# Performance work log

Measured on AMD Instinct MI355X. Metric: run time of the kernel, lower is better.

The kernel has to match this reference:

```python
import jax, jax.numpy as jnp
import numpy as np

N, M, NNZ, D, H = 4096, 1024, 65536, 512, 8
DH = D // H
DFF = 4 * D
EPS = 1e-5


def layer_norm(x, g, b):
    mu = jnp.mean(x, axis=-1, keepdims=True)
    var = jnp.mean((x - mu) ** 2, axis=-1, keepdims=True)
    return (x - mu) / jnp.sqrt(var + EPS) * g + b


def setup_inputs() -> dict:
    key = jax.random.key(0)
    ks = jax.random.split(key, 16)
    s = 1.0 / np.sqrt(D)
    inp = {}
    inp['x'] = jax.random.normal(ks[0], (N, D), jnp.float32)
    node = jax.random.randint(ks[1], (NNZ,), 0, N, jnp.int32)
    edge = jax.random.randint(ks[2], (NNZ,), 0, M, jnp.int32)
    inp['hyperedge_index'] = jnp.stack([node, edge], axis=0)
    inp['hyperedge_attr'] = jax.random.normal(ks[3], (M, D), jnp.float32)
    # HypergraphConv params (heads=1): lin (no bias), att [2*D], output bias
    inp['Wh'] = jax.random.normal(ks[4], (D, D), jnp.float32) * s
    inp['att'] = jax.random.normal(ks[5], (2 * D,), jnp.float32) * s
    inp['bias_h'] = jnp.zeros((D,), jnp.float32)
    # outer LayerNorms
    inp['ln1_g'] = jnp.ones((D,), jnp.float32); inp['ln1_b'] = jnp.zeros((D,), jnp.float32)
    inp['ln2_g'] = jnp.ones((D,), jnp.float32); inp['ln2_b'] = jnp.zeros((D,), jnp.float32)
    # TransformerEncoderLayer params (post-norm, relu, dropout off at eval)
    inp['in_proj_w'] = jax.random.normal(ks[6], (3 * D, D), jnp.float32) * s
    inp['in_proj_b'] = jnp.zeros((3 * D,), jnp.float32)
    inp['out_proj_w'] = jax.random.normal(ks[7], (D, D), jnp.float32) * s
    inp['out_proj_b'] = jnp.zeros((D,), jnp.float32)
    inp['ff1_w'] = jax.random.normal(ks[8], (DFF, D), jnp.float32) * s
    inp['ff1_b'] = jnp.zeros((DFF,), jnp.float32)
    inp['ff2_w'] = jax.random.normal(ks[9], (D, DFF), jnp.float32) * (1.0 / np.sqrt(DFF))
    inp['ff2_b'] = jnp.zeros((D,), jnp.float32)
    inp['tln1_g'] = jnp.ones((D,), jnp.float32); inp['tln1_b'] = jnp.zeros((D,), jnp.float32)
    inp['tln2_g'] = jnp.ones((D,), jnp.float32); inp['tln2_b'] = jnp.zeros((D,), jnp.float32)
    return inp


def hypergraph_conv(x, node, edge, hyperedge_attr, Wh, att, bias_h):
    # PyG HypergraphConv, use_attention=True, heads=1, concat=True
    xl = x @ Wh.T                      # [N, D]
    el = hyperedge_attr @ Wh.T         # [M, D]
    # per-incidence attention score
    a = xl[node] @ att[:D] + el[edge] @ att[D:]          # [NNZ]
    a = jnp.where(a >= 0, a, 0.2 * a)                    # leaky_relu(0.2)
    # scatter-softmax grouped by node index
    amax = jax.ops.segment_max(a, node, num_segments=N)
    a = jnp.exp(a - amax[node])
    den = jax.ops.segment_sum(a, node, num_segments=N)
    alpha = a / (den[node] + 1e-16)
    # degree normalizations (hyperedge_weight = ones)
    ones = jnp.ones((NNZ,), x.dtype)
    Dn = jax.ops.segment_sum(ones, node, num_segments=N)
    Dinv = jnp.where(Dn > 0, 1.0 / Dn, 0.0)
    Bn = jax.ops.segment_sum(ones, edge, num_segments=M)
    Binv = jnp.where(Bn > 0, 1.0 / Bn, 0.0)
    # node -> hyperedge aggregation
    msg1 = (Binv[edge] * alpha)[:, None] * xl[node]      # [NNZ, D]
    ef = jax.ops.segment_sum(msg1, edge, num_segments=M)  # [M, D]
    # hyperedge -> node aggregation
    msg2 = (Dinv[node] * alpha)[:, None] * ef[edge]
    out = jax.ops.segment_sum(msg2, node, num_segments=N)  # [N, D]
    return out + bias_h


def reference(x, hyperedge_index, hyperedge_attr, Wh, att, bias_h,
              ln1_g, ln1_b, ln2_g, ln2_b,
              in_proj_w, in_proj_b, out_proj_w, out_proj_b,
              ff1_w, ff1_b, ff2_w, ff2_b,
              tln1_g, tln1_b, tln2_g, tln2_b):
    node, edge = hyperedge_index[0], hyperedge_index[1]
    x_conv = hypergraph_conv(x, node, edge, hyperedge_attr, Wh, att, bias_h)
    x1 = layer_norm(x + x_conv, ln1_g, ln1_b)
    # TransformerEncoderLayer (post-norm, eval: dropout off), seq of N tokens
    qkv = x1 @ in_proj_w.T + in_proj_b
    q, k, v = jnp.split(qkv, 3, axis=-1)
    q = q.reshape(N, H, DH); k = k.reshape(N, H, DH); v = v.reshape(N, H, DH)
    scores = jnp.einsum('nhd,mhd->hnm', q, k) / np.sqrt(DH)
    attw = jax.nn.softmax(scores, axis=-1)
    ctx = jnp.einsum('hnm,mhd->nhd', attw, v).reshape(N, D)
    attn_out = ctx @ out_proj_w.T + out_proj_b
    x2 = layer_norm(x1 + attn_out, tln1_g, tln1_b)
    ff = jax.nn.relu(x2 @ ff1_w.T + ff1_b) @ ff2_w.T + ff2_b
    x3 = layer_norm(x2 + ff, tln2_g, tln2_b)
    return layer_norm(x1 + x3, ln2_g, ln2_b)
```

## Files before the change

kernel.cpp:

```cpp
#include <hip/hip_runtime.h>
#include <math.h>

#define NN   4096
#define MM   1024
#define NNZC 65536
#define DD   512
#define HH   8
#define DHH  64
#define DFFC 2048
#define NSPLIT 4

typedef short bf16x8 __attribute__((ext_vector_type(8)));
typedef float f32x4  __attribute__((ext_vector_type(4)));

static __device__ inline unsigned short f2bf(float f) {
  union { float f; unsigned int u; } v; v.f = f;
  unsigned int r = v.u + 0x7fff + ((v.u >> 16) & 1);
  return (unsigned short)(r >> 16);
}
static __device__ inline float bf2f(unsigned short u) {
  return __uint_as_float((unsigned int)u << 16);
}

__device__ inline void gload16(const void* g, void* l) {
  __builtin_amdgcn_global_load_lds(
      (const __attribute__((address_space(1))) void*)g,
      (__attribute__((address_space(3))) void*)l, 16, 0, 0);
}

__device__ inline void atomicMaxF(float* addr, float val) {
  if (val >= 0.f) atomicMax((int*)addr, __float_as_int(val));
  else            atomicMin((unsigned int*)addr, __float_as_uint(val));
}

__global__ void init_kernel(float* amax, float* den, int* DnCnt, int* BnCnt,
                            int* node_cur, int* edge_cur) {
  int i = blockIdx.x * 256 + threadIdx.x;
  if (i < NN) { amax[i] = -INFINITY; den[i] = 0.f; DnCnt[i] = 0; node_cur[i] = 0; }
  if (i < MM) { BnCnt[i] = 0; edge_cur[i] = 0; }
}

__global__ __launch_bounds__(256) void f2b_multi(
    const float* s0, unsigned short* d0, int n0,
    const float* s1, unsigned short* d1, int n1,
    const float* s2, unsigned short* d2, int n2,
    const float* s3, unsigned short* d3, int n3,
    const float* s4, unsigned short* d4, int n4,
    const float* s5, unsigned short* d5, int n5,
    const float* s6, unsigned short* d6, int n6) {
  const float* in; unsigned short* out; int n8;
  switch (blockIdx.y) {
    case 0: in=s0; out=d0; n8=n0; break;
    case 1: in=s1; out=d1; n8=n1; break;
    case 2: in=s2; out=d2; n8=n2; break;
    case 3: in=s3; out=d3; n8=n3; break;
    case 4: in=s4; out=d4; n8=n4; break;
    case 5: in=s5; out=d5; n8=n5; break;
    default: in=s6; out=d6; n8=n6; break;
  }
  for (int i = blockIdx.x*256 + threadIdx.x; i < n8; i += gridDim.x*256) {
    float4 v0 = *(const float4*)&in[(size_t)i*8];
    float4 v1 = *(const float4*)&in[(size_t)i*8 + 4];
    unsigned short w[8];
    w[0]=f2bf(v0.x); w[1]=f2bf(v0.y); w[2]=f2bf(v0.z); w[3]=f2bf(v0.w);
    w[4]=f2bf(v1.x); w[5]=f2bf(v1.y); w[6]=f2bf(v1.z); w[7]=f2bf(v1.w);
    *(ulonglong2*)&out[(size_t)i*8] = *(ulonglong2*)w;
  }
}

__global__ __launch_bounds__(256) void gemm_bt_bf16(
    const unsigned short* __restrict__ A, const unsigned short* __restrict__ B,
    const float* __restrict__ bias, float* __restrict__ Cf,
    unsigned short* __restrict__ Cb, int N, int K, int relu) {
  __shared__ __align__(16) unsigned short Al[128*64];
  __shared__ __align__(16) unsigned short Bl[128*64];
  const int t = threadIdx.x;
  const int w = t >> 6, l = t & 63;
  const int lg = l >> 4, lid = l & 15;
  const int wr = w >> 1, wc = w & 1;
  const int bm = blockIdx.x * 128, bn = blockIdx.y * 128;

  f32x4 acc[4][4];
  #pragma unroll
  for (int mi = 0; mi < 4; ++mi)
    #pragma unroll
    for (int ni = 0; ni < 4; ++ni) acc[mi][ni] = (f32x4)0.f;

  for (int k0 = 0; k0 < K; k0 += 64) {
    #pragma unroll
    for (int i = 0; i < 4; ++i) {
      int cid = i*256 + t;
      int row = cid >> 3, cp = cid & 7;
      int gc = cp ^ (row & 7);
      gload16(&A[(size_t)(bm + row)*K + k0 + gc*8], &Al[cid*8]);
      gload16(&B[(size_t)(bn + row)*K + k0 + gc*8], &Bl[cid*8]);
    }
    asm volatile("s_waitcnt vmcnt(0)" ::: "memory");
    __syncthreads();
    #pragma unroll
    for (int ks = 0; ks < 2; ++ks) {
      bf16x8 af[4], bfr[4];
      #pragma unroll
      for (int mi = 0; mi < 4; ++mi) {
        int r = wr*64 + mi*16 + lid;
        af[mi] = *(const bf16x8*)&Al[r*64 + ((ks*4 + lg) ^ (r & 7))*8];
      }
      #pragma unroll
      for (int ni = 0; ni < 4; ++ni) {
        int r = wc*64 + ni*16 + lid;
        bfr[ni] = *(const bf16x8*)&Bl[r*64 + ((ks*4 + lg) ^ (r & 7))*8];
      }
      __builtin_amdgcn_s_setprio(1);
      #pragma unroll
      for (int mi = 0; mi < 4; ++mi)
        #pragma unroll
        for (int ni = 0; ni < 4; ++ni)
          acc[mi][ni] = __builtin_amdgcn_mfma_f32_16x16x32_bf16(af[mi], bfr[ni], acc[mi][ni], 0, 0, 0);
      __builtin_amdgcn_s_setprio(0);
    }
    __syncthreads();
  }

  #pragma unroll
  for (int ni = 0; ni < 4; ++ni) {
    int col = bn + wc*64 + ni*16 + lid;
    float bv = bias ? bias[col] : 0.f;
    #pragma unroll
    for (int mi = 0; mi < 4; ++mi) {
      #pragma unroll
      for (int rg = 0; rg < 4; ++rg) {
        int row = bm + wr*64 + mi*16 + lg*4 + rg;
        float v = acc[mi][ni][rg] + bv;
        if (relu) v = fmaxf(v, 0.f);
        if (Cf) Cf[(size_t)row*N + col] = v;
        if (Cb) Cb[(size_t)row*N + col] = f2bf(v);
      }
    }
  }
}

__global__ __launch_bounds__(256) void gemm_bt_bf16_n64(
    const unsigned short* __restrict__ A, const unsigned short* __restrict__ B,
    const float* __restrict__ bias, unsigned short* __restrict__ Cb, int N, int K) {
  __shared__ __align__(16) unsigned short Al[128*64];
  __shared__ __align__(16) unsigned short Bl[64*64];
  const int t = threadIdx.x;
  const int w = t >> 6, l = t & 63;
  const int lg = l >> 4, lid = l & 15;
  const int wr = w >> 1, wc = w & 1;
  const int bm = blockIdx.x * 128, bn = blockIdx.y * 64;

  f32x4 acc[4][2];
  #pragma unroll
  for (int mi = 0; mi < 4; ++mi)
    #pragma unroll
    for (int ni = 0; ni < 2; ++ni) acc[mi][ni] = (f32x4)0.f;

  for (int k0 = 0; k0 < K; k0 += 64) {
    #pragma unroll
    for (int i = 0; i < 4; ++i) {
      int cid = i*256 + t;
      int row = cid >> 3, cp = cid & 7;
      int gc = cp ^ (row & 7);
      gload16(&A[(size_t)(bm + row)*K + k0 + gc*8], &Al[cid*8]);
    }
    #pragma unroll
    for (int i = 0; i < 2; ++i) {
      int cid = i*256 + t;
      int row = cid >> 3, cp = cid & 7;
      int gc = cp ^ (row & 7);
      gload16(&B[(size_t)(bn + row)*K + k0 + gc*8], &Bl[cid*8]);
    }
    asm volatile("s_waitcnt vmcnt(0)" ::: "memory");
    __syncthreads();
    #pragma unroll
    for (int ks = 0; ks < 2; ++ks) {
      bf16x8 af[4], bfr[2];
      #pragma unroll
      for (int mi = 0; mi < 4; ++mi) {
        int r = wr*64 + mi*16 + lid;
        af[mi] = *(const bf16x8*)&Al[r*64 + ((ks*4 + lg) ^ (r & 7))*8];
      }
      #pragma unroll
      for (int ni = 0; ni < 2; ++ni) {
        int r = wc*32 + ni*16 + lid;
        bfr[ni] = *(const bf16x8*)&Bl[r*64 + ((ks*4 + lg) ^ (r & 7))*8];
      }
      __builtin_amdgcn_s_setprio(1);
      #pragma unroll
      for (int mi = 0; mi < 4; ++mi)
        #pragma unroll
        for (int ni = 0; ni < 2; ++ni)
          acc[mi][ni] = __builtin_amdgcn_mfma_f32_16x16x32_bf16(af[mi], bfr[ni], acc[mi][ni], 0, 0, 0);
      __builtin_amdgcn_s_setprio(0);
    }
    __syncthreads();
  }

  #pragma unroll
  for (int ni = 0; ni < 2; ++ni) {
    int col = bn + wc*32 + ni*16 + lid;
    float bv = bias ? bias[col] : 0.f;
    #pragma unroll
    for (int mi = 0; mi < 4; ++mi) {
      #pragma unroll
      for (int rg = 0; rg < 4; ++rg) {
        int row = bm + wr*64 + mi*16 + lg*4 + rg;
        Cb[(size_t)row*N + col] = f2bf(acc[mi][ni][rg] + bv);
      }
    }
  }
}

__global__ __launch_bounds__(256) void rowdot_b16(const unsigned short* __restrict__ X,
    const float* __restrict__ vec, float* __restrict__ out, int rows) {
  int w = (blockIdx.x * 256 + threadIdx.x) >> 6;
  int lane = threadIdx.x & 63;
  if (w >= rows) return;
  const unsigned short* xr = &X[(size_t)w * DD];
  float s = 0.f;
  #pragma unroll
  for (int j = 0; j < 8; ++j) s += bf2f(xr[lane + 64*j]) * vec[lane + 64*j];
  #pragma unroll
  for (int off = 1; off < 64; off <<= 1) s += __shfl_xor(s, off, 64);
  if (lane == 0) out[w] = s;
}

__global__ void incidence_pass1(const int* __restrict__ node_idx, const int* __restrict__ edge_idx,
    const float* __restrict__ s_node, const float* __restrict__ s_edge,
    float* __restrict__ a_buf, float* amax, int* DnCnt, int* BnCnt) {
  int i = blockIdx.x * 256 + threadIdx.x;
  if (i >= NNZC) return;
  int n = node_idx[i], m = edge_idx[i];
  float a = s_node[n] + s_edge[m];
  a = (a >= 0.f) ? a : 0.2f * a;
  a_buf[i] = a;
  atomicMaxF(&amax[n], a);
  atomicAdd(&DnCnt[n], 1);
  atomicAdd(&BnCnt[m], 1);
}

__global__ __launch_bounds__(1024) void exscan_kernel(const int* __restrict__ in,
                                                      int* __restrict__ out, int n) {
  __shared__ int sums[1024];
  const int t = threadIdx.x;
  const int chunk = (n + 1023) >> 10;
  const int start = t * chunk;
  const int stop  = min(start + chunk, n);
  int local = 0;
  for (int i = start; i < stop; ++i) local += in[i];
  sums[t] = local;
  __syncthreads();
  for (int o = 1; o < 1024; o <<= 1) {
    int v = (t >= o) ? sums[t - o] : 0;
    __syncthreads();
    sums[t] += v;
    __syncthreads();
  }
  int run = (t == 0) ? 0 : sums[t - 1];
  for (int i = start; i < stop; ++i) { out[i] = run; run += in[i]; }
  if (t == 1023) out[n] = sums[1023];
}

__global__ void incidence_pass2(const int* __restrict__ node_idx, const int* __restrict__ edge_idx,
    float* __restrict__ a_buf, const float* __restrict__ amax, float* den,
    const int* __restrict__ node_off, const int* __restrict__ edge_off,
    int* node_cur, int* edge_cur, int* node_list, int* edge_list) {
  int i = blockIdx.x * 256 + threadIdx.x;
  if (i >= NNZC) return;
  int n = node_idx[i], m = edge_idx[i];
  float e = __expf(a_buf[i] - amax[n]);
  a_buf[i] = e;
  atomicAdd(&den[n], e);
  int pn = atomicAdd(&node_cur[n], 1);
  node_list[node_off[n] + pn] = i;
  int pm = atomicAdd(&edge_cur[m], 1);
  edge_list[edge_off[m] + pm] = i;
}

__global__ __launch_bounds__(256) void gather_edge(const int* __restrict__ edge_off,
    const int* __restrict__ edge_list, const int* __restrict__ node_idx,
    const float* __restrict__ a_buf, const float* __restrict__ den,
    const unsigned short* __restrict__ xlb, unsigned short* __restrict__ efb) {
  int m = blockIdx.x;
  int t = threadIdx.x;
  int beg = edge_off[m], end = edge_off[m+1];
  int cnt = end - beg;
  float Binv = (cnt > 0) ? (1.0f / (float)cnt) : 0.f;
  __shared__ int   ln_[128];
  __shared__ float lw_[128];
  float acc0 = 0.f, acc1 = 0.f;
  for (int c = beg; c < end; c += 128) {
    int nchunk = min(128, end - c);
    if (t < nchunk) {
      int i = edge_list[c + t];
      int n = node_idx[i];
      ln_[t] = n;
      lw_[t] = a_buf[i] / (den[n] + 1e-16f) * Binv;
    }
    __syncthreads();
    float a0 = 0.f, a1 = 0.f, b0 = 0.f, b1 = 0.f;
    int j = 0;
    for (; j + 1 < nchunk; j += 2) {
      float w0 = lw_[j], w1 = lw_[j+1];
      const unsigned short* r0 = &xlb[(size_t)ln_[j]   * DD];
      const unsigned short* r1 = &xlb[(size_t)ln_[j+1] * DD];
      a0 += w0 * bf2f(r0[t]);       b0 += w0 * bf2f(r0[t + 256]);
      a1 += w1 * bf2f(r1[t]);       b1 += w1 * bf2f(r1[t + 256]);
    }
    if (j < nchunk) {
      float w0 = lw_[j];
      const unsigned short* r0 = &xlb[(size_t)ln_[j] * DD];
      a0 += w0 * bf2f(r0[t]);       b0 += w0 * bf2f(r0[t + 256]);
    }
    acc0 += a0 + a1;
    acc1 += b0 + b1;
    __syncthreads();
  }
  efb[(size_t)m * DD + t]       = f2bf(acc0);
  efb[(size_t)m * DD + t + 256] = f2bf(acc1);
}

__global__ __launch_bounds__(256) void gather_node(const int* __restrict__ node_off,
    const int* __restrict__ node_list, const int* __restrict__ edge_idx,
    const float* __restrict__ a_buf, const float* __restrict__ den,
    const unsigned short* __restrict__ efb, const float* __restrict__ bias_h,
    float* __restrict__ conv) {
  int n = blockIdx.x;
  int t = threadIdx.x;
  int beg = node_off[n], end = node_off[n+1];
  int cnt = end - beg;
  float Dinv = (cnt > 0) ? (1.0f / (float)cnt) : 0.f;
  float wscale = Dinv / (den[n] + 1e-16f);
  __shared__ int   le_[128];
  __shared__ float lw_[128];
  float acc0 = 0.f, acc1 = 0.f;
  for (int c = beg; c < end; c += 128) {
    int nchunk = min(128, end - c);
    if (t < nchunk) {
      int i = node_list[c + t];
      le_[t] = edge_idx[i];
      lw_[t] = a_buf[i] * wscale;
    }
    __syncthreads();
    float a0 = 0.f, a1 = 0.f, b0 = 0.f, b1 = 0.f;
    int j = 0;
    for (; j + 1 < nchunk; j += 2) {
      float w0 = lw_[j], w1 = lw_[j+1];
      const unsigned short* r0 = &efb[(size_t)le_[j]   * DD];
      const unsigned short* r1 = &efb[(size_t)le_[j+1] * DD];
      a0 += w0 * bf2f(r0[t]);       b0 += w0 * bf2f(r0[t + 256]);
      a1 += w1 * bf2f(r1[t]);       b1 += w1 * bf2f(r1[t + 256]);
    }
    if (j < nchunk) {
      float w0 = lw_[j];
      const unsigned short* r0 = &efb[(size_t)le_[j] * DD];
      a0 += w0 * bf2f(r0[t]);       b0 += w0 * bf2f(r0[t + 256]);
    }
    acc0 += a0 + a1;
    acc1 += b0 + b1;
    __syncthreads();
  }
  conv[(size_t)n * DD + t]       = acc0 + bias_h[t];
  conv[(size_t)n * DD + t + 256] = acc1 + bias_h[t + 256];
}

__global__ __launch_bounds__(256) void ln_residual(const float* __restrict__ a,
    const float* __restrict__ b, const unsigned short* __restrict__ bB,
    const float* __restrict__ g, const float* __restrict__ be,
    float* __restrict__ out, unsigned short* __restrict__ outb) {
  int r = blockIdx.x;
  int t = threadIdx.x;
  float b0 = b ? b[(size_t)r*DD + t]       : bf2f(bB[(size_t)r*DD + t]);
  float b1 = b ? b[(size_t)r*DD + t + 256] : bf2f(bB[(size_t)r*DD + t + 256]);
  float v0 = a[(size_t)r*DD + t]       + b0;
  float v1 = a[(size_t)r*DD + t + 256] + b1;
  __shared__ float red[4];
  __shared__ float mu_s, rstd_s;
  float s = v0 + v1;
  #pragma unroll
  for (int off = 1; off < 64; off <<= 1) s += __shfl_xor(s, off, 64);
  int wid = t >> 6;
  if ((t & 63) == 0) red[wid] = s;
  __syncthreads();
  if (t == 0) mu_s = (red[0] + red[1] + red[2] + red[3]) / 512.f;
  __syncthreads();
  float mu = mu_s;
  float d0 = v0 - mu, d1 = v1 - mu;
  float vs = d0*d0 + d1*d1;
  #pragma unroll
  for (int off = 1; off < 64; off <<= 1) vs += __shfl_xor(vs, off, 64);
  if ((t & 63) == 0) red[wid] = vs;
  __syncthreads();
  if (t == 0) rstd_s = rsqrtf((red[0] + red[1] + red[2] + red[3]) / 512.f + 1e-5f);
  __syncthreads();
  float rs = rstd_s;
  float o0 = d0 * rs * g[t]       + be[t];
  float o1 = d1 * rs * g[t + 256] + be[t + 256];
  out[(size_t)r*DD + t]       = o0;
  out[(size_t)r*DD + t + 256] = o1;
  if (outb) {
    outb[(size_t)r*DD + t]       = f2bf(o0);
    outb[(size_t)r*DD + t + 256] = f2bf(o1);
  }
}

__global__ __launch_bounds__(256) void ln_final2(const float* __restrict__ x2,
    const unsigned short* __restrict__ ffob, const float* __restrict__ x1,
    const float* __restrict__ g1, const float* __restrict__ b1,
    const float* __restrict__ g2, const float* __restrict__ b2,
    float* __restrict__ out) {
  int r = blockIdx.x;
  int t = threadIdx.x;
  __shared__ float red[4];
  __shared__ float sh0, sh1;
  int wid = t >> 6;
  float v0 = x2[(size_t)r*DD + t]       + bf2f(ffob[(size_t)r*DD + t]);
  float v1 = x2[(size_t)r*DD + t + 256] + bf2f(ffob[(size_t)r*DD + t + 256]);
  float s = v0 + v1;
  #pragma unroll
  for (int off = 1; off < 64; off <<= 1) s += __shfl_xor(s, off, 64);
  if ((t & 63) == 0) red[wid] = s;
  __syncthreads();
  if (t == 0) sh0 = (red[0] + red[1] + red[2] + red[3]) / 512.f;
  __syncthreads();
  float mu = sh0;
  float d0 = v0 - mu, d1 = v1 - mu;
  float vs = d0*d0 + d1*d1;
  #pragma unroll
  for (int off = 1; off < 64; off <<= 1) vs += __shfl_xor(vs, off, 64);
  if ((t & 63) == 0) red[wid] = vs;
  __syncthreads();
  if (t == 0) sh1 = rsqrtf((red[0] + red[1] + red[2] + red[3]) / 512.f + 1e-5f);
  __syncthreads();
  float rs = sh1;
  float x30 = d0 * rs * g1[t]       + b1[t];
  float x31 = d1 * rs * g1[t + 256] + b1[t + 256];
  __syncthreads();
  float u0 = x1[(size_t)r*DD + t]       + x30;
  float u1 = x1[(size_t)r*DD + t + 256] + x31;
  s = u0 + u1;
  #pragma unroll
  for (int off = 1; off < 64; off <<= 1) s += __shfl_xor(s, off, 64);
  if ((t & 63) == 0) red[wid] = s;
  __syncthreads();
  if (t == 0) sh0 = (red[0] + red[1] + red[2] + red[3]) / 512.f;
  __syncthreads();
  mu = sh0;
  d0 = u0 - mu; d1 = u1 - mu;
  vs = d0*d0 + d1*d1;
  #pragma unroll
  for (int off = 1; off < 64; off <<= 1) vs += __shfl_xor(vs, off, 64);
  if ((t & 63) == 0) red[wid] = vs;
  __syncthreads();
  if (t == 0) sh1 = rsqrtf((red[0] + red[1] + red[2] + red[3]) / 512.f + 1e-5f);
  __syncthreads();
  rs = sh1;
  out[(size_t)r*DD + t]       = d0 * rs * g2[t]       + b2[t];
  out[(size_t)r*DD + t + 256] = d1 * rs * g2[t + 256] + b2[t + 256];
}

__global__ __launch_bounds__(256) void conv_vt(const unsigned short* __restrict__ qkvbb,
                                               unsigned short* __restrict__ Vtb) {
  __shared__ unsigned short Tl[64][76];
  const int h = blockIdx.y;
  const int tt = blockIdx.x * 64;
  const int t = threadIdx.x;
  {
    int row = t >> 2;
    int cbase = (t & 3) * 16;
    const unsigned short* src = &qkvbb[(size_t)(tt + row)*1536 + 1024 + h*64];
    #pragma unroll
    for (int jj = 0; jj < 4; ++jj)
      *(ushort4*)&Tl[row][cbase + jj*4] = *(const ushort4*)&src[cbase + jj*4];
  }
  __syncthreads();
  #pragma unroll
  for (int it = 0; it < 4; ++it) {
    int d = it*16 + (t >> 4);
    int tk = (t & 15) * 4;
    ushort4 w4;
    w4.x = Tl[tk+0][d]; w4.y = Tl[tk+1][d]; w4.z = Tl[tk+2][d]; w4.w = Tl[tk+3][d];
    *(ushort4*)&Vtb[(size_t)h*64*NN + (size_t)d*NN + tt + tk] = w4;
  }
}

__global__ __launch_bounds__(256) void attn_mfma_part(const unsigned short* __restrict__ qkvbb,
                                                      const unsigned short* __restrict__ Vtb,
                                                      unsigned short* __restrict__ Opartb,
                                                      float* __restrict__ ml) {
  const int head = blockIdx.y;
  const int z = blockIdx.z;
  const int q0 = blockIdx.x * 64;
  const int t = threadIdx.x;
  const int w = t >> 6;
  const int l = t & 63;
  const int lg = l >> 4;
  const int lid = l & 15;
  const float sc = 0.125f * 1.44269504f;
  const float THRraw = 44.36f;

  __shared__ __align__(16) unsigned short Kl[64*64];
  __shared__ __align__(16) unsigned short Vl[64*64];

  bf16x8 qa[2];
  {
    const int qrow = q0 + w*16 + lid;
    const unsigned short* qp = &qkvbb[(size_t)qrow*1536 + head*64];
    qa[0] = *(const bf16x8*)&qp[lg*8];
    qa[1] = *(const bf16x8*)&qp[32 + lg*8];
  }

  float m = -1e30f, msc = -1e30f, lsum = 0.f;
  f32x4 o[4];
  #pragma unroll
  for (int dt = 0; dt < 4; ++dt) o[dt] = (f32x4)0.f;

  const unsigned short* Kh = qkvbb + 512 + head*64;
  const unsigned short* Vh = Vtb + (size_t)head*64*NN;
  const int kt0 = z * (NN / NSPLIT);
  const int kt1 = kt0 + (NN / NSPLIT);

  const int srow0 = t >> 3,        scc = (t & 7) * 8;
  const int srow1 = 32 + (t >> 3);
  const int sdst0 = (srow0*64 + scc) ^ ((srow0 & 7) << 3);
  const int sdst1 = (srow1*64 + scc) ^ ((srow1 & 7) << 3);
  const int kperm0 = 8*((srow0>>2)&3) + 4*((srow0>>4)&1) + (srow0&3) + 32*(srow0>>5);
  const int kperm1 = 8*((srow1>>2)&3) + 4*((srow1>>4)&1) + (srow1&3) + 32*(srow1>>5);
  ulonglong2 kreg0, kreg1, vreg0, vreg1;

#define LOADKV(ktv) do { \
    kreg0 = *(const ulonglong2*)&Kh[(size_t)((ktv) + kperm0)*1536 + scc]; \
    vreg0 = *(const ulonglong2*)&Vh[(size_t)srow0*NN + (ktv) + scc]; \
    kreg1 = *(const ulonglong2*)&Kh[(size_t)((ktv) + kperm1)*1536 + scc]; \
    vreg1 = *(const ulonglong2*)&Vh[(size_t)srow1*NN + (ktv) + scc]; \
  } while (0)
#define STORKV() do { \
    *(ulonglong2*)&Kl[sdst0] = kreg0; *(ulonglong2*)&Vl[sdst0] = vreg0; \
    *(ulonglong2*)&Kl[sdst1] = kreg1; *(ulonglong2*)&Vl[sdst1] = vreg1; \
  } while (0)

  LOADKV(kt0);
  STORKV();
  __syncthreads();

  for (int kt = kt0; kt < kt1; kt += 64) {
    const bool hn = (kt + 64) < kt1;
    if (hn) LOADKV(kt + 64);

    f32x4 s[4];
    #pragma unroll
    for (int n = 0; n < 4; ++n) s[n] = (f32x4)0.f;
    __builtin_amdgcn_s_setprio(1);
    #pragma unroll
    for (int n = 0; n < 4; ++n) {
      int tok = n*16 + lid;
      #pragma unroll
      for (int hf = 0; hf < 2; ++hf) {
        int didx = (tok*64 + hf*32 + lg*8) ^ ((tok & 7) << 3);
        bf16x8 kb = *(const bf16x8*)&Kl[didx];
        s[n] = __builtin_amdgcn_mfma_f32_16x16x32_bf16(kb, qa[hf], s[n], 0, 0, 0);
      }
    }
    __builtin_amdgcn_s_setprio(0);

    float a0 = fmaxf(fmaxf(s[0][0], s[0][1]), s[0][2]);
    float a1 = fmaxf(fmaxf(s[0][3], s[1][0]), s[1][1]);
    float a2 = fmaxf(fmaxf(s[1][2], s[1][3]), s[2][0]);
    float a3 = fmaxf(fmaxf(s[2][1], s[2][2]), s[2][3]);
    float a4 = fmaxf(fmaxf(s[3][0], s[3][1]), s[3][2]);
    float mx = fmaxf(fmaxf(fmaxf(a0, a1), a2), fmaxf(fmaxf(a3, a4), s[3][3]));
    mx = fmaxf(mx, __shfl_xor(mx, 16, 64));
    mx = fmaxf(mx, __shfl_xor(mx, 32, 64));
    if (!__all(mx <= m + THRraw)) {
      float mn = fmaxf(m, mx);
      float c = exp2f((m - mn) * sc);
      m = mn;
      msc = m * sc;
      lsum *= c;
      #pragma unroll
      for (int r = 0; r < 4; ++r) {
        float cr = __shfl(c, lg*4 + r, 64);
        #pragma unroll
        for (int dt = 0; dt < 4; ++dt) o[dt][r] *= cr;
      }
    }
    float ps = 0.f;
    #pragma unroll
    for (int n = 0; n < 4; ++n)
      #pragma unroll
      for (int r = 0; r < 4; ++r) {
        float p = exp2f(fmaf(s[n][r], sc, -msc));
        s[n][r] = p;
        ps += p;
      }
    ps += __shfl_xor(ps, 16, 64);
    ps += __shfl_xor(ps, 32, 64);
    lsum += ps;

    union { bf16x8 v; unsigned int u[4]; } pa[2];
    #pragma unroll
    for (int hf = 0; hf < 2; ++hf) {
      asm("v_cvt_pk_bf16_f32 %0, %1, %2" : "=v"(pa[hf].u[0]) : "v"(s[2*hf][0]),   "v"(s[2*hf][1]));
      asm("v_cvt_pk_bf16_f32 %0, %1, %2" : "=v"(pa[hf].u[1]) : "v"(s[2*hf][2]),   "v"(s[2*hf][3]));
      asm("v_cvt_pk_bf16_f32 %0, %1, %2" : "=v"(pa[hf].u[2]) : "v"(s[2*hf+1][0]), "v"(s[2*hf+1][1]));
      asm("v_cvt_pk_bf16_f32 %0, %1, %2" : "=v"(pa[hf].u[3]) : "v"(s[2*hf+1][2]), "v"(s[2*hf+1][3]));
    }

    __builtin_amdgcn_s_setprio(1);
    #pragma unroll
    for (int dt = 0; dt < 4; ++dt) {
      int drow = dt*16 + lid;
      #pragma unroll
      for (int hf = 0; hf < 2; ++hf) {
        int didx = (drow*64 + hf*32 + lg*8) ^ ((drow & 7) << 3);
        bf16x8 vb = *(const bf16x8*)&Vl[didx];
        o[dt] = __builtin_amdgcn_mfma_f32_16x16x32_bf16(pa[hf].v, vb, o[dt], 0, 0, 0);
      }
    }
    __builtin_amdgcn_s_setprio(0);

    __syncthreads();
    if (hn) {
      STORKV();
      __syncthreads();
    }
  }
#undef LOADKV
#undef STORKV

  #pragma unroll
  for (int r = 0; r < 4; ++r) {
    int q = q0 + w*16 + lg*4 + r;
    size_t base = ((size_t)(z*HH + head)*NN + q)*64;
    #pragma unroll
    for (int dt = 0; dt < 4; ++dt)
      Opartb[base + dt*16 + lid] = f2bf(o[dt][r]);
  }
  if (l < 16) {
    int q = q0 + w*16 + l;
    size_t mb = ((size_t)(z*HH + head)*NN + q)*2;
    ml[mb]     = msc;
    ml[mb + 1] = lsum;
  }
}

__global__ __launch_bounds__(256) void attn_combine(const unsigned short* __restrict__ Opartb,
                                                    const float* __restrict__ ml,
                                                    unsigned short* __restrict__ ctxb) {
  const int w = threadIdx.x >> 6, lane = threadIdx.x & 63;
  const int row = blockIdx.x * 4 + w;
  const int q = row >> 3, head = row & 7;
  float ms[NSPLIT], ls[NSPLIT];
  float mglob = -1e30f;
  #pragma unroll
  for (int s = 0; s < NSPLIT; ++s) {
    size_t mb = ((size_t)(s*HH + head)*NN + q)*2;
    ms[s] = ml[mb]; ls[s] = ml[mb + 1];
    mglob = fmaxf(mglob, ms[s]);
  }
  float lt = 0.f, ov = 0.f;
  #pragma unroll
  for (int s = 0; s < NSPLIT; ++s) {
    float wgt = exp2f(ms[s] - mglob);
    lt += ls[s] * wgt;
    ov += bf2f(Opartb[((size_t)(s*HH + head)*NN + q)*64 + lane]) * wgt;
  }
  ctxb[(size_t)q*DD + head*64 + lane] = f2bf(ov / lt);
}

extern "C" void kernel_launch(void* const* d_in, const int* in_sizes, int n_in,
                              void* d_out, int out_size, void* d_ws, size_t ws_size,
                              hipStream_t stream) {
  const float* x       = (const float*)d_in[0];
  const int*   hidx    = (const int*)d_in[1];
  const float* hattr   = (const float*)d_in[2];
  const float* Wh      = (const float*)d_in[3];
  const float* att     = (const float*)d_in[4];
  const float* bias_h  = (const float*)d_in[5];
  const float* ln1_g   = (const float*)d_in[6];
  const float* ln1_b   = (const float*)d_in[7];
  const float* ln2_g   = (const float*)d_in[8];
  const float* ln2_b   = (const float*)d_in[9];
  const float* in_proj_w  = (const float*)d_in[10];
  const float* in_proj_b  = (const float*)d_in[11];
  const float* out_proj_w = (const float*)d_in[12];
  const float* out_proj_b = (const float*)d_in[13];
  const float* ff1_w   = (const float*)d_in[14];
  const float* ff1_b   = (const float*)d_in[15];
  const float* ff2_w   = (const float*)d_in[16];
  const float* ff2_b   = (const float*)d_in[17];
  const float* tln1_g  = (const float*)d_in[18];
  const float* tln1_b  = (const float*)d_in[19];
  const float* tln2_g  = (const float*)d_in[20];
  const float* tln2_b  = (const float*)d_in[21];
  const int* node_idx = hidx;
  const int* edge_idx = hidx + NNZC;

  char* ws = (char*)d_ws;
  size_t off = 0;
  auto alloc = [&](size_t bytes) -> void* {
    void* p = ws + off;
    off = (off + bytes + 63) & ~(size_t)63;
    return p;
  };
  float* s_node   = (float*)alloc(sizeof(float)*NN);
  float* s_edge   = (float*)alloc(sizeof(float)*MM);
  float* a_buf    = (float*)alloc(sizeof(float)*NNZC);
  float* amax     = (float*)alloc(sizeof(float)*NN);
  float* den      = (float*)alloc(sizeof(float)*NN);
  int*   DnCnt    = (int*)alloc(sizeof(int)*NN);
  int*   BnCnt    = (int*)alloc(sizeof(int)*MM);
  int*   node_off = (int*)alloc(sizeof(int)*(NN+1));
  int*   edge_off = (int*)alloc(sizeof(int)*(MM+1));
  int*   node_cur = (int*)alloc(sizeof(int)*NN);
  int*   edge_cur = (int*)alloc(sizeof(int)*MM);
  int*   node_list= (int*)alloc(sizeof(int)*NNZC);
  int*   edge_list= (int*)alloc(sizeof(int)*NNZC);
  float* conv     = (float*)alloc(sizeof(float)*NN*DD);
  float* x1       = (float*)alloc(sizeof(float)*NN*DD);
  float* x2       = (float*)alloc(sizeof(float)*NN*DD);
  unsigned short* xhb   = (unsigned short*)alloc(sizeof(unsigned short)*(NN+MM)*DD);
  unsigned short* xelb  = (unsigned short*)alloc(sizeof(unsigned short)*(NN+MM)*DD);
  unsigned short* efb   = (unsigned short*)alloc(sizeof(unsigned short)*MM*DD);
  unsigned short* qkvbb = (unsigned short*)alloc(sizeof(unsigned short)*NN*3*DD);
  unsigned short* Vtb   = (unsigned short*)alloc(sizeof(unsigned short)*NN*DD);
  unsigned short* Whb   = (unsigned short*)alloc(sizeof(unsigned short)*DD*DD);
  unsigned short* ipwb  = (unsigned short*)alloc(sizeof(unsigned short)*3*DD*DD);
  unsigned short* opwb  = (unsigned short*)alloc(sizeof(unsigned short)*DD*DD);
  unsigned short* ff1wb = (unsigned short*)alloc(sizeof(unsigned short)*DFFC*DD);
  unsigned short* ff2wb = (unsigned short*)alloc(sizeof(unsigned short)*DD*DFFC);
  unsigned short* x1b   = (unsigned short*)alloc(sizeof(unsigned short)*NN*DD);
  unsigned short* x2b   = (unsigned short*)alloc(sizeof(unsigned short)*NN*DD);
  unsigned short* ctxb  = (unsigned short*)alloc(sizeof(unsigned short)*NN*DD);
  unsigned short* attn_outb = (unsigned short*)alloc(sizeof(unsigned short)*NN*DD);
  char* late = (char*)alloc(20u*1024*1024);
  unsigned short* Opartb = (unsigned short*)late;
  float*          mlb    = (float*)(late + 16u*1024*1024);
  unsigned short* ffhb   = (unsigned short*)late;
  unsigned short* ffob   = (unsigned short*)(late + 16u*1024*1024);
  unsigned short* xlb = xelb;
  unsigned short* elb = xelb + (size_t)NN*DD;
  (void)ws_size; (void)in_sizes; (void)n_in; (void)out_size;

  dim3 b256(256);
  f2b_multi<<<dim3(256, 7), b256, 0, stream>>>(
      x, xhb, NN*DD/8,  hattr, xhb + (size_t)NN*DD, MM*DD/8,  Wh, Whb, DD*DD/8,
      in_proj_w, ipwb, 3*DD*DD/8,  out_proj_w, opwb, DD*DD/8,
      ff1_w, ff1wb, DFFC*DD/8,  ff2_w, ff2wb, DD*DFFC/8);

  gemm_bt_bf16_n64<<<dim3((NN+MM)/128, DD/64), b256, 0, stream>>>(xhb, Whb, nullptr, xelb, DD, DD);
  rowdot_b16<<<NN/4, b256, 0, stream>>>(xlb, att,      s_node, NN);
  rowdot_b16<<<MM/4, b256, 0, stream>>>(elb, att + DD, s_edge, MM);
  init_kernel<<<NN/256, b256, 0, stream>>>(amax, den, DnCnt, BnCnt, node_cur, edge_cur);
  incidence_pass1<<<NNZC/256, b256, 0, stream>>>(node_idx, edge_idx, s_node, s_edge,
                                                 a_buf, amax, DnCnt, BnCnt);
  exscan_kernel<<<1, 1024, 0, stream>>>(DnCnt, node_off, NN);
  exscan_kernel<<<1, 1024, 0, stream>>>(BnCnt, edge_off, MM);
  incidence_pass2<<<NNZC/256, b256, 0, stream>>>(node_idx, edge_idx, a_buf, amax, den,
                                                 node_off, edge_off, node_cur, edge_cur,
                                                 node_list, edge_list);
  gather_edge<<<MM, b256, 0, stream>>>(edge_off, edge_list, node_idx, a_buf, den, xlb, efb);
  gather_node<<<NN, b256, 0, stream>>>(node_off, node_list, edge_idx, a_buf, den, efb, bias_h, conv);
  ln_residual<<<NN, b256, 0, stream>>>(x, conv, nullptr, ln1_g, ln1_b, x1, x1b);
  gemm_bt_bf16_n64<<<dim3(NN/128, (3*DD)/64), b256, 0, stream>>>(x1b, ipwb, in_proj_b, qkvbb, 3*DD, DD);
  conv_vt<<<dim3(NN/64, HH), b256, 0, stream>>>(qkvbb, Vtb);
  attn_mfma_part<<<dim3(NN/64, HH, NSPLIT), b256, 0, stream>>>(qkvbb, Vtb, Opartb, mlb);
  attn_combine<<<NN*HH/4, b256, 0, stream>>>(Opartb, mlb, ctxb);
  gemm_bt_bf16_n64<<<dim3(NN/128, DD/64), b256, 0, stream>>>(ctxb, opwb, out_proj_b, attn_outb, DD, DD);
  ln_residual<<<NN, b256, 0, stream>>>(x1, nullptr, attn_outb, tln1_g, tln1_b, x2, x2b);
  gemm_bt_bf16<<<dim3(NN/128, DFFC/128), b256, 0, stream>>>(x2b, ff1wb, ff1_b, nullptr, ffhb, DFFC, DD, 1);
  gemm_bt_bf16_n64<<<dim3(NN/128, DD/64), b256, 0, stream>>>(ffhb, ff2wb, ff2_b, ffob, DD, DFFC);
  ln_final2<<<NN, b256, 0, stream>>>(x2, ffob, x1, tln2_g, tln2_b, ln2_g, ln2_b, (float*)d_out);
}
```

Measured before the change: 278.6 us.

## Fuse small launches, merge LayerNorm into gather, and widen attention key tile

Merges the two rowdot launches and the two exclusive-scan launches into single launches, and fuses the first residual LayerNorm into the node gather kernel, which removes the fp32 conv intermediate buffer. The flash-attention part kernel now processes 128 keys per iteration instead of 64, doubling the K/V shared-memory tiles and per-iteration MFMA work. These cut launch overhead, a full-tensor round trip through memory, and per-tile loop and synchronisation costs. The trade-off is higher register and LDS use in the attention kernel, which may reduce occupancy.

After: 343.2 us. +23.2%, slower.

```diff
diff --git a/kernel.cpp b/kernel.cpp
--- a/kernel.cpp
+++ b/kernel.cpp
@@ -212,18 +212,24 @@
   }
 }
 
-__global__ __launch_bounds__(256) void rowdot_b16(const unsigned short* __restrict__ X,
-    const float* __restrict__ vec, float* __restrict__ out, int rows) {
+__global__ __launch_bounds__(256) void rowdot_both(const unsigned short* __restrict__ xlb,
+    const unsigned short* __restrict__ elb, const float* __restrict__ att,
+    float* __restrict__ s_node, float* __restrict__ s_edge) {
   int w = (blockIdx.x * 256 + threadIdx.x) >> 6;
   int lane = threadIdx.x & 63;
-  if (w >= rows) return;
-  const unsigned short* xr = &X[(size_t)w * DD];
+  const unsigned short* xr;
+  const float* vec;
+  if (w < NN) { xr = &xlb[(size_t)w * DD]; vec = att; }
+  else        { xr = &elb[(size_t)(w - NN) * DD]; vec = att + DD; }
   float s = 0.f;
   #pragma unroll
   for (int j = 0; j < 8; ++j) s += bf2f(xr[lane + 64*j]) * vec[lane + 64*j];
   #pragma unroll
   for (int off = 1; off < 64; off <<= 1) s += __shfl_xor(s, off, 64);
-  if (lane == 0) out[w] = s;
+  if (lane == 0) {
+    if (w < NN) s_node[w] = s;
+    else        s_edge[w - NN] = s;
+  }
 }
 
 __global__ void incidence_pass1(const int* __restrict__ node_idx, const int* __restrict__ edge_idx,
@@ -240,8 +246,11 @@
   atomicAdd(&BnCnt[m], 1);
 }
 
-__global__ __launch_bounds__(1024) void exscan_kernel(const int* __restrict__ in,
-                                                      int* __restrict__ out, int n) {
+__global__ __launch_bounds__(1024) void exscan2_kernel(const int* __restrict__ inA,
+    int* __restrict__ outA, int nA, const int* __restrict__ inB, int* __restrict__ outB, int nB) {
+  const int* in; int* out; int n;
+  if (blockIdx.x == 0) { in = inA; out = outA; n = nA; }
+  else                 { in = inB; out = outB; n = nB; }
   __shared__ int sums[1024];
   const int t = threadIdx.x;
   const int chunk = (n + 1023) >> 10;
@@ -321,11 +330,12 @@
   efb[(size_t)m * DD + t + 256] = f2bf(acc1);
 }
 
-__global__ __launch_bounds__(256) void gather_node(const int* __restrict__ node_off,
+__global__ __launch_bounds__(256) void gather_node_ln(const int* __restrict__ node_off,
     const int* __restrict__ node_list, const int* __restrict__ edge_idx,
     const float* __restrict__ a_buf, const float* __restrict__ den,
     const unsigned short* __restrict__ efb, const float* __restrict__ bias_h,
-    float* __restrict__ conv) {
+    const float* __restrict__ x, const float* __restrict__ g, const float* __restrict__ be,
+    float* __restrict__ x1, unsigned short* __restrict__ x1b) {
   int n = blockIdx.x;
   int t = threadIdx.x;
   int beg = node_off[n], end = node_off[n+1];
@@ -361,8 +371,34 @@
     acc1 += b0 + b1;
     __syncthreads();
   }
-  conv[(size_t)n * DD + t]       = acc0 + bias_h[t];
-  conv[(size_t)n * DD + t + 256] = acc1 + bias_h[t + 256];
+  float v0 = x[(size_t)n*DD + t]       + acc0 + bias_h[t];
+  float v1 = x[(size_t)n*DD + t + 256] + acc1 + bias_h[t + 256];
+  __shared__ float red[4];
+  __shared__ float mu_s, rstd_s;
+  float s = v0 + v1;
+  #pragma unroll
+  for (int off = 1; off < 64; off <<= 1) s += __shfl_xor(s, off, 64);
+  int wid = t >> 6;
+  if ((t & 63) == 0) red[wid] = s;
+  __syncthreads();
+  if (t == 0) mu_s = (red[0] + red[1] + red[2] + red[3]) / 512.f;
+  __syncthreads();
+  float mu = mu_s;
+  float d0 = v0 - mu, d1 = v1 - mu;
+  float vs = d0*d0 + d1*d1;
+  #pragma unroll
+  for (int off = 1; off < 64; off <<= 1) vs += __shfl_xor(vs, off, 64);
+  if ((t & 63) == 0) red[wid] = vs;
+  __syncthreads();
+  if (t == 0) rstd_s = rsqrtf((red[0] + red[1] + red[2] + red[3]) / 512.f + 1e-5f);
+  __syncthreads();
+  float rs = rstd_s;
+  float o0 = d0 * rs * g[t]       + be[t];
+  float o1 = d1 * rs * g[t + 256] + be[t + 256];
+  x1[(size_t)n*DD + t]        = o0;
+  x1[(size_t)n*DD + t + 256]  = o1;
+  x1b[(size_t)n*DD + t]       = f2bf(o0);
+  x1b[(size_t)n*DD + t + 256] = f2bf(o1);
 }
 
 __global__ __launch_bounds__(256) void ln_residual(const float* __restrict__ a,
@@ -500,8 +536,8 @@
   const float sc = 0.125f * 1.44269504f;
   const float THRraw = 44.36f;
 
-  __shared__ __align__(16) unsigned short Kl[64*64];
-  __shared__ __align__(16) unsigned short Vl[64*64];
+  __shared__ __align__(16) unsigned short Kl[128*64];
+  __shared__ __align__(16) unsigned short Vl[64*128];
 
   bf16x8 qa[2];
   {
@@ -521,39 +557,56 @@
   const int kt0 = z * (NN / NSPLIT);
   const int kt1 = kt0 + (NN / NSPLIT);
 
-  const int srow0 = t >> 3,        scc = (t & 7) * 8;
-  const int srow1 = 32 + (t >> 3);
-  const int sdst0 = (srow0*64 + scc) ^ ((srow0 & 7) << 3);
-  const int sdst1 = (srow1*64 + scc) ^ ((srow1 & 7) << 3);
-  const int kperm0 = 8*((srow0>>2)&3) + 4*((srow0>>4)&1) + (srow0&3) + 32*(srow0>>5);
-  const int kperm1 = 8*((srow1>>2)&3) + 4*((srow1>>4)&1) + (srow1&3) + 32*(srow1>>5);
-  ulonglong2 kreg0, kreg1, vreg0, vreg1;
+  int krow[4], kdst[4], kprm[4], vrow[4], vcp[4], vdst[4];
+  #pragma unroll
+  for (int i = 0; i < 4; ++i) {
+    int kc = i*256 + t;
+    krow[i] = kc >> 3;
+    int cp = kc & 7;
+    kdst[i] = (krow[i]*64 + cp*8) ^ ((krow[i] & 7) << 3);
+    int r = krow[i] & 63;
+    kprm[i] = 8*((r>>2)&3) + 4*((r>>4)&1) + (r&3) + 32*(r>>5) + (krow[i] & 64);
+    kprm[i] = kprm[i];
+    kdst[i] = kdst[i];
+    kprm[i] = kprm[i] | (cp << 16);
+    int vc = i*256 + t;
+    vrow[i] = vc >> 4;
+    vcp[i]  = vc & 15;
+    vdst[i] = (vrow[i]*128 + vcp[i]*8) ^ ((vrow[i] & 7) << 3);
+  }
+  ulonglong2 kreg[4], vreg[4];
 
 #define LOADKV(ktv) do { \
-    kreg0 = *(const ulonglong2*)&Kh[(size_t)((ktv) + kperm0)*1536 + scc]; \
-    vreg0 = *(const ulonglong2*)&Vh[(size_t)srow0*NN + (ktv) + scc]; \
-    kreg1 = *(const ulonglong2*)&Kh[(size_t)((ktv) + kperm1)*1536 + scc]; \
-    vreg1 = *(const ulonglong2*)&Vh[(size_t)srow1*NN + (ktv) + scc]; \
+    _Pragma("unroll") \
+    for (int i = 0; i < 4; ++i) { \
+      int tokp = (ktv) + (kprm[i] & 0xffff); \
+      int cp = kprm[i] >> 16; \
+      kreg[i] = *(const ulonglong2*)&Kh[(size_t)tokp*1536 + cp*8]; \
+      vreg[i] = *(const ulonglong2*)&Vh[(size_t)vrow[i]*NN + (ktv) + vcp[i]*8]; \
+    } \
   } while (0)
 #define STORKV() do { \
-    *(ulonglong2*)&Kl[sdst0] = kreg0; *(ulonglong2*)&Vl[sdst0] = vreg0; \
-    *(ulonglong2*)&Kl[sdst1] = kreg1; *(ulonglong2*)&Vl[sdst1] = vreg1; \
+    _Pragma("unroll") \
+    for (int i = 0; i < 4; ++i) { \
+      *(ulonglong2*)&Kl[kdst[i]] = kreg[i]; \
+      *(ulonglong2*)&Vl[vdst[i]] = vreg[i]; \
+    } \
   } while (0)
 
   LOADKV(kt0);
   STORKV();
   __syncthreads();
 
-  for (int kt = kt0; kt < kt1; kt += 64) {
-    const bool hn = (kt + 64) < kt1;
-    if (hn) LOADKV(kt + 64);
-
-    f32x4 s[4];
-    #pragma unroll
-    for (int n = 0; n < 4; ++n) s[n] = (f32x4)0.f;
+  for (int kt = kt0; kt < kt1; kt += 128) {
+    const bool hn = (kt + 128) < kt1;
+    if (hn) LOADKV(kt + 128);
+
+    f32x4 s[8];
+    #pragma unroll
+    for (int n = 0; n < 8; ++n) s[n] = (f32x4)0.f;
     __builtin_amdgcn_s_setprio(1);
     #pragma unroll
-    for (int n = 0; n < 4; ++n) {
+    for (int n = 0; n < 8; ++n) {
       int tok = n*16 + lid;
       #pragma unroll
       for (int hf = 0; hf < 2; ++hf) {
@@ -564,12 +617,11 @@
     }
     __builtin_amdgcn_s_setprio(0);
 
-    float a0 = fmaxf(fmaxf(s[0][0], s[0][1]), s[0][2]);
-    float a1 = fmaxf(fmaxf(s[0][3], s[1][0]), s[1][1]);
-    float a2 = fmaxf(fmaxf(s[1][2], s[1][3]), s[2][0]);
-    float a3 = fmaxf(fmaxf(s[2][1], s[2][2]), s[2][3]);
-    float a4 = fmaxf(fmaxf(s[3][0], s[3][1]), s[3][2]);
-    float mx = fmaxf(fmaxf(fmaxf(a0, a1), a2), fmaxf(fmaxf(a3, a4), s[3][3]));
+    float mx = s[0][0];
+    #pragma unroll
+    for (int n = 0; n < 8; ++n)
+      #pragma unroll
+      for (int r = 0; r < 4; ++r) mx = fmaxf(mx, s[n][r]);
     mx = fmaxf(mx, __shfl_xor(mx, 16, 64));
     mx = fmaxf(mx, __shfl_xor(mx, 32, 64));
     if (!__all(mx <= m + THRraw)) {
@@ -587,7 +639,7 @@
     }
     float ps = 0.f;
     #pragma unroll
-    for (int n = 0; n < 4; ++n)
+    for (int n = 0; n < 8; ++n)
       #pragma unroll
       for (int r = 0; r < 4; ++r) {
         float p = exp2f(fmaf(s[n][r], sc, -msc));
@@ -598,13 +650,13 @@
     ps += __shfl_xor(ps, 32, 64);
     lsum += ps;
 
-    union { bf16x8 v; unsigned int u[4]; } pa[2];
-    #pragma unroll
-    for (int hf = 0; hf < 2; ++hf) {
-      asm("v_cvt_pk_bf16_f32 %0, %1, %2" : "=v"(pa[hf].u[0]) : "v"(s[2*hf][0]),   "v"(s[2*hf][1]));
-      asm("v_cvt_pk_bf16_f32 %0, %1, %2" : "=v"(pa[hf].u[1]) : "v"(s[2*hf][2]),   "v"(s[2*hf][3]));
-      asm("v_cvt_pk_bf16_f32 %0, %1, %2" : "=v"(pa[hf].u[2]) : "v"(s[2*hf+1][0]), "v"(s[2*hf+1][1]));
-      asm("v_cvt_pk_bf16_f32 %0, %1, %2" : "=v"(pa[hf].u[3]) : "v"(s[2*hf+1][2]), "v"(s[2*hf+1][3]));
+    union { bf16x8 v; unsigned int u[4]; } pa[4];
+    #pragma unroll
+    for (int g = 0; g < 4; ++g) {
+      asm("v_cvt_pk_bf16_f32 %0, %1, %2" : "=v"(pa[g].u[0]) : "v"(s[2*g][0]),   "v"(s[2*g][1]));
+      asm("v_cvt_pk_bf16_f32 %0, %1, %2" : "=v"(pa[g].u[1]) : "v"(s[2*g][2]),   "v"(s[2*g][3]));
+      asm("v_cvt_pk_bf16_f32 %0, %1, %2" : "=v"(pa[g].u[2]) : "v"(s[2*g+1][0]), "v"(s[2*g+1][1]));
+      asm("v_cvt_pk_bf16_f32 %0, %1, %2" : "=v"(pa[g].u[3]) : "v"(s[2*g+1][2]), "v"(s[2*g+1][3]));
     }
 
     __builtin_amdgcn_s_setprio(1);
@@ -612,10 +664,10 @@
     for (int dt = 0; dt < 4; ++dt) {
       int drow = dt*16 + lid;
       #pragma unroll
-      for (int hf = 0; hf < 2; ++hf) {
-        int didx = (drow*64 + hf*32 + lg*8) ^ ((drow & 7) << 3);
+      for (int g = 0; g < 4; ++g) {
+        int didx = (drow*128 + g*32 + lg*8) ^ ((drow & 7) << 3);
         bf16x8 vb = *(const bf16x8*)&Vl[didx];
-        o[dt] = __builtin_amdgcn_mfma_f32_16x16x32_bf16(pa[hf].v, vb, o[dt], 0, 0, 0);
+        o[dt] = __builtin_amdgcn_mfma_f32_16x16x32_bf16(pa[g].v, vb, o[dt], 0, 0, 0);
       }
     }
     __builtin_amdgcn_s_setprio(0);
@@ -717,7 +769,6 @@
   int*   edge_cur = (int*)alloc(sizeof(int)*MM);
   int*   node_list= (int*)alloc(sizeof(int)*NNZC);
   int*   edge_list= (int*)alloc(sizeof(int)*NNZC);
-  float* conv     = (float*)alloc(sizeof(float)*NN*DD);
   float* x1       = (float*)alloc(sizeof(float)*NN*DD);
   float* x2       = (float*)alloc(sizeof(float)*NN*DD);
   unsigned short* xhb   = (unsigned short*)alloc(sizeof(unsigned short)*(NN+MM)*DD);
@@ -750,19 +801,17 @@
       ff1_w, ff1wb, DFFC*DD/8,  ff2_w, ff2wb, DD*DFFC/8);
 
   gemm_bt_bf16_n64<<<dim3((NN+MM)/128, DD/64), b256, 0, stream>>>(xhb, Whb, nullptr, xelb, DD, DD);
-  rowdot_b16<<<NN/4, b256, 0, stream>>>(xlb, att,      s_node, NN);
-  rowdot_b16<<<MM/4, b256, 0, stream>>>(elb, att + DD, s_edge, MM);
+  rowdot_both<<<(NN+MM)/4, b256, 0, stream>>>(xlb, elb, att, s_node, s_edge);
   init_kernel<<<NN/256, b256, 0, stream>>>(amax, den, DnCnt, BnCnt, node_cur, edge_cur);
   incidence_pass1<<<NNZC/256, b256, 0, stream>>>(node_idx, edge_idx, s_node, s_edge,
                                                  a_buf, amax, DnCnt, BnCnt);
-  exscan_kernel<<<1, 1024, 0, stream>>>(DnCnt, node_off, NN);
-  exscan_kernel<<<1, 1024, 0, stream>>>(BnCnt, edge_off, MM);
+  exscan2_kernel<<<2, 1024, 0, stream>>>(DnCnt, node_off, NN, BnCnt, edge_off, MM);
   incidence_pass2<<<NNZC/256, b256, 0, stream>>>(node_idx, edge_idx, a_buf, amax, den,
                                                  node_off, edge_off, node_cur, edge_cur,
                                                  node_list, edge_list);
   gather_edge<<<MM, b256, 0, stream>>>(edge_off, edge_list, node_idx, a_buf, den, xlb, efb);
-  gather_node<<<NN, b256, 0, stream>>>(node_off, node_list, edge_idx, a_buf, den, efb, bias_h, conv);
-  ln_residual<<<NN, b256, 0, stream>>>(x, conv, nullptr, ln1_g, ln1_b, x1, x1b);
+  gather_node_ln<<<NN, b256, 0, stream>>>(node_off, node_list, edge_idx, a_buf, den, efb,
+                                          bias_h, x, ln1_g, ln1_b, x1, x1b);
   gemm_bt_bf16_n64<<<dim3(NN/128, (3*DD)/64), b256, 0, stream>>>(x1b, ipwb, in_proj_b, qkvbb, 3*DD, DD);
   conv_vt<<<dim3(NN/64, HH), b256, 0, stream>>>(qkvbb, Vtb);
   attn_mfma_part<<<dim3(NN/64, HH, NSPLIT), b256, 0, stream>>>(qkvbb, Vtb, Opartb, mlb);
```
